# Kernel optimization log

Hardware: AMD Instinct MI355X
Metric: run time of the kernel (lower is better)

Reference implementation:

```python
import jax, jax.numpy as jnp
import numpy as np

B, K, W = 16, 64, 2048
D, DH, DFF, NL, V = 512, 256, 2048, 4, 32001
LN_EPS = 1e-5


def _ln(x, g, b):
    mu = jnp.mean(x, axis=-1, keepdims=True)
    var = jnp.mean(jnp.square(x - mu), axis=-1, keepdims=True)
    return (x - mu) * jax.lax.rsqrt(var + LN_EPS) * g + b


def setup_inputs() -> dict:
    key = jax.random.key(0)
    ks = iter(jax.random.split(key, 64))
    nrm = lambda shape, s=0.02: (jax.random.normal(next(ks), shape, dtype=jnp.float32) * s)
    inp = {
        "cache": jax.random.randint(next(ks), (B, K), 0, V),
        "seq": jax.random.randint(next(ks), (B, W), 0, V),
        "item_embed": nrm((V, D)),
        "cache_pos_embed": nrm((K, D)),
        "seq_pos_embed": nrm((W, D)),
        "segment_embed": nrm((2, D)),
        # per-layer stacked params (leading dim NL)
        "wq_s": nrm((NL, D, DH)), "wk_s": nrm((NL, D, DH)), "wv_s": nrm((NL, D, DH)),
        "wq_c": nrm((NL, D, DH)), "wk_c": nrm((NL, D, DH)), "wv_c": nrm((NL, D, DH)),
        "w_out": nrm((NL, D, D)), "b_out": jnp.zeros((NL, D), jnp.float32),
        "ln1_g": jnp.ones((NL, D), jnp.float32), "ln1_b": jnp.zeros((NL, D), jnp.float32),
        "ln2_g": jnp.ones((NL, D), jnp.float32), "ln2_b": jnp.zeros((NL, D), jnp.float32),
        "w_ff1": nrm((NL, D, DFF)), "b_ff1": jnp.zeros((NL, DFF), jnp.float32),
        "w_ff2": nrm((NL, DFF, D)), "b_ff2": jnp.zeros((NL, D), jnp.float32),
        "fin_g": jnp.ones((D,), jnp.float32), "fin_b": jnp.zeros((D,), jnp.float32),
        "w_ev": nrm((D, 1)), "b_ev": jnp.zeros((1,), jnp.float32),
    }
    return inp


def _forward(cache, seq, item_embed, cache_pos_embed, seq_pos_embed, segment_embed,
             wq_s, wk_s, wv_s, wq_c, wk_c, wv_c, w_out, b_out,
             ln1_g, ln1_b, ln2_g, ln2_b, w_ff1, b_ff1, w_ff2, b_ff2,
             fin_g, fin_b, w_ev, b_ev):
    scale = 1.0 / jnp.sqrt(jnp.float32(DH))
    cache_emb = item_embed[cache] + cache_pos_embed[None, :, :] + segment_embed[0]
    seq_emb = item_embed[seq] + seq_pos_embed[None, :, :] + segment_embed[1]
    h = jnp.concatenate([cache_emb, seq_emb], axis=1)  # (B, K+W, D)
    L = K + W
    # additive mask for stream a: cache rows attend to all seq tokens,
    # seq rows are causal within the window.  (L, W)
    causal = jnp.triu(jnp.full((W, W), -jnp.inf, dtype=jnp.float32), k=1)
    mask_a = jnp.concatenate([jnp.zeros((K, W), jnp.float32), causal], axis=0)

    for l in range(NL):
        hn = _ln(h, ln1_g[l], ln1_b[l])
        hn_seq = hn[:, K:]
        hn_cache = hn[:, :K]
        # stream a: all tokens query the sequence window (causal for seq rows)
        q_a = hn @ wq_s[l]
        k_a = hn_seq @ wk_s[l]
        v_a = hn_seq @ wv_s[l]
        scores_a = jnp.einsum('bld,bwd->blw', q_a, k_a) * scale + mask_a
        out_a = jnp.einsum('blw,bwd->bld', jax.nn.softmax(scores_a, axis=-1), v_a)
        # stream b: all tokens query the cache slots (full attention)
        q_b = hn @ wq_c[l]
        k_b = hn_cache @ wk_c[l]
        v_b = hn_cache @ wv_c[l]
        scores_b = jnp.einsum('bld,bkd->blk', q_b, k_b) * scale
        out_b = jnp.einsum('blk,bkd->bld', jax.nn.softmax(scores_b, axis=-1), v_b)
        attn_out = jnp.concatenate([out_a, out_b], axis=-1)  # (B, L, D)
        h = h + attn_out @ w_out[l] + b_out[l]
        hn2 = _ln(h, ln2_g[l], ln2_b[l])
        h = h + jax.nn.relu(hn2 @ w_ff1[l] + b_ff1[l]) @ w_ff2[l] + b_ff2[l]

    h = _ln(h, fin_g, fin_b)
    logits = (h[:, :K] @ w_ev + b_ev)[..., 0]  # (B, K)
    return logits


def reference(cache, seq, item_embed, cache_pos_embed, seq_pos_embed, segment_embed,
              wq_s, wk_s, wv_s, wq_c, wk_c, wv_c, w_out, b_out,
              ln1_g, ln1_b, ln2_g, ln2_b, w_ff1, b_ff1, w_ff2, b_ff2,
              fin_g, fin_b, w_ev, b_ev):
    return _forward(cache, seq, item_embed, cache_pos_embed, seq_pos_embed, segment_embed,
                    wq_s, wk_s, wv_s, wq_c, wk_c, wv_c, w_out, b_out,
                    ln1_g, ln1_b, ln2_g, ln2_b, w_ff1, b_ff1, w_ff2, b_ff2,
                    fin_g, fin_b, w_ev, b_ev)
```

## Files before the change

### kernel.cpp

```cpp
#include <hip/hip_runtime.h>
#include <hip/hip_bf16.h>
#include <cstdint>

#define CB 16
#define CK 64
#define CW 2048
#define CL 2112
#define CD 512
#define CDH 256
#define CDFF 2048
#define CNL 4
#define CROWS (CB*CL)
#define NCH 2
#define RCH2 (CROWS/NCH)

typedef __attribute__((ext_vector_type(8))) short bf16x8;
typedef __attribute__((ext_vector_type(4))) float f32x4;

__device__ __forceinline__ float bf2f(unsigned short u) {
    union { unsigned int i; float f; } x; x.i = ((unsigned int)u) << 16; return x.f;
}

__device__ __forceinline__ void load_lds16(const void* g, void* l) {
    __builtin_amdgcn_global_load_lds(
        (const __attribute__((address_space(1))) void*)g,
        (__attribute__((address_space(3))) void*)l, 16, 0, 0);
}

__device__ __forceinline__ void xcd_swizzle(int& bx, int& by) {
    const int gx = gridDim.x, nwg = gx * gridDim.y;
    if ((nwg & 7) == 0) {
        const int flat = by * gx + bx;
        const int cpx = nwg >> 3;
        const int swz = (flat & 7) * cpx + (flat >> 3);
        bx = swz % gx; by = swz / gx;
    }
}

#define BM 128
#define BN 128
#define BKG 64

__global__ __launch_bounds__(256) void gemm_bt(
    const short* __restrict__ A, const short* __restrict__ Bt, void* __restrict__ C,
    const float* __restrict__ bias, int M, int N, int Kd,
    int lda, int ldb, int ldc, long sA, long sB, long sC, float scale, int epi,
    int ksplit)
{
    __shared__ short lA[2][BM * BKG];
    __shared__ short lB[2][BN * BKG];
    const int tid = threadIdx.x;
    const int wave = tid >> 6, lane = tid & 63;
    const int wy = wave >> 1, wx = wave & 1;
    const int lr = lane & 15, quad = lane >> 4;
    int bx = blockIdx.x, by = blockIdx.y;
    xcd_swizzle(bx, by);
    const int m0 = by * BM, n0 = bx * BN;
    const int z = blockIdx.z;
    const short* Ab = A + (size_t)z * sA;
    const short* Bb = Bt + (size_t)z * sB;

    f32x4 acc[4][4];
#pragma unroll
    for (int i = 0; i < 4; i++)
#pragma unroll
        for (int j = 0; j < 4; j++) acc[i][j] = (f32x4){0.f, 0.f, 0.f, 0.f};

    const int sRow = lane >> 3;
    const int sCol = (((lane & 7) ^ sRow) << 3);

    int kbeg = 0, kend = Kd;
    if (ksplit > 1) { const int kc = Kd / ksplit; kbeg = z * kc; kend = kbeg + kc; }
    const int nsteps = (kend - kbeg) / BKG;

    auto stage = [&](int buf, int k0) {
#pragma unroll
        for (int n = 0; n < 4; ++n) {
            const int c = wave * 4 + n;
            int ar = m0 + c * 8 + sRow; if (ar > M - 1) ar = M - 1;
            load_lds16(Ab + (size_t)ar * lda + k0 + sCol, &lA[buf][c * 512]);
            int br = n0 + c * 8 + sRow; if (br > N - 1) br = N - 1;
            load_lds16(Bb + (size_t)br * ldb + k0 + sCol, &lB[buf][c * 512]);
        }
    };

    stage(0, kbeg);
    for (int t = 0; t < nsteps; ++t) {
        const int cur = t & 1;
        if (t + 1 < nsteps) {
            stage(cur ^ 1, kbeg + (t + 1) * BKG);
            asm volatile("s_waitcnt vmcnt(8)\n\ts_barrier" ::: "memory");
        } else {
            asm volatile("s_waitcnt vmcnt(0)\n\ts_barrier" ::: "memory");
        }
#pragma unroll
        for (int kk = 0; kk < BKG; kk += 32) {
            const int k4 = kk >> 3;
            bf16x8 av[4], bv[4];
#pragma unroll
            for (int i = 0; i < 4; i++) {
                const int ri = wy * 64 + i * 16 + lr;
                av[i] = *(const bf16x8*)&lA[cur][ri * BKG + ((((k4 + quad) ^ (ri & 7)) << 3))];
            }
#pragma unroll
            for (int j = 0; j < 4; j++) {
                const int rj = wx * 64 + j * 16 + lr;
                bv[j] = *(const bf16x8*)&lB[cur][rj * BKG + ((((k4 + quad) ^ (rj & 7)) << 3))];
            }
#pragma unroll
            for (int i = 0; i < 4; i++)
#pragma unroll
                for (int j = 0; j < 4; j++)
                    acc[i][j] = __builtin_amdgcn_mfma_f32_16x16x32_bf16(av[i], bv[j], acc[i][j], 0, 0, 0);
        }
        asm volatile("s_barrier" ::: "memory");
    }

    const int colBase = n0 + wx * 64 + lr;
    if (epi == 3) {
        float* Cp = (float*)C + (size_t)z * sC;
#pragma unroll
        for (int i = 0; i < 4; i++) {
            const int row0 = m0 + wy * 64 + i * 16 + quad * 4;
#pragma unroll
            for (int j = 0; j < 4; j++) {
                const int col = colBase + j * 16;
                if (col >= N) continue;
                const float bv_ = bias ? bias[col] : 0.f;
#pragma unroll
                for (int r = 0; r < 4; r++) {
                    const int row = row0 + r;
                    if (row < M) Cp[(size_t)row * ldc + col] += acc[i][j][r] + bv_;
                }
            }
        }
    } else {
        __hip_bfloat16* Cp = (__hip_bfloat16*)C + (size_t)z * sC;
#pragma unroll
        for (int i = 0; i < 4; i++) {
            const int row0 = m0 + wy * 64 + i * 16 + quad * 4;
#pragma unroll
            for (int j = 0; j < 4; j++) {
                const int col = colBase + j * 16;
                if (col >= N) continue;
                const float bv_ = (epi == 1) ? bias[col] : 0.f;
#pragma unroll
                for (int r = 0; r < 4; r++) {
                    const int row = row0 + r;
                    if (row < M) {
                        float v = acc[i][j][r];
                        if (epi == 1) { v += bv_; v = v > 0.f ? v : 0.f; }
                        else if (epi == 2) v *= scale;
                        Cp[(size_t)row * ldc + col] = __float2bfloat16(v);
                    }
                }
            }
        }
    }
}

__global__ __launch_bounds__(256, 2) void flash_a(
    const short* __restrict__ q,
    const short* __restrict__ ka,
    const short* __restrict__ vt,
    short* __restrict__ out)
{
    __shared__ short kbuf[64 * 256];
    __shared__ short vbuf[256 * 64];
    __shared__ short pbuf[64 * 64];
    const int tid = threadIdx.x, wave = tid >> 6, lane = tid & 63;
    const int lr = lane & 15, quad = lane >> 4;

    const int id = blockIdx.x;
    const int x = id & 7, k = id >> 3;
    const int b = 2 * x + (k >= 33);
    const int mi = (k >= 33) ? (k - 33) : k;
    const int mt = (mi == 0) ? 0 : (33 - mi);
    const int m0 = mt * 64;
    const short* kab = ka + (size_t)b * 2048 * 256;
    const short* vtb = vt + (size_t)b * 256 * 2048;

    const int nkt = (mt == 0) ? 32 : mt;

    bf16x8 qf[8];
    {
        const int qr = m0 + wave * 16 + lr;
        const short* p0 = q + ((size_t)b * CL + qr) * 512;
#pragma unroll
        for (int s = 0; s < 8; ++s) qf[s] = *(const bf16x8*)(p0 + s * 32 + quad * 8);
    }

    auto stageK = [&](int kt) {
#pragma unroll
        for (int u = 0; u < 8; ++u) {
            const int seg = u * 4 + wave;
            const int idx = seg * 64 + lane;
            const int row = idx >> 5, cp = idx & 31;
            const int cs = cp ^ (row & 7);
            load_lds16(kab + (size_t)(kt * 64 + row) * 256 + cs * 8, kbuf + seg * 512);
        }
    };
    auto stageV = [&](int kt) {
#pragma unroll
        for (int u = 0; u < 8; ++u) {
            const int seg = u * 4 + wave;
            const int idx = seg * 64 + lane;
            const int row = idx >> 3, cp = idx & 7;
            const int cs = cp ^ (row & 7);
            load_lds16(vtb + (size_t)row * 2048 + kt * 64 + cs * 8, vbuf + seg * 512);
        }
    };

    f32x4 acc_o[16];
#pragma unroll
    for (int jd = 0; jd < 16; jd++) acc_o[jd] = (f32x4){0.f, 0.f, 0.f, 0.f};
    float m_run[4], l_run[4];
    int limit[4];
#pragma unroll
    for (int rr = 0; rr < 4; rr++) {
        m_run[rr] = -1e30f; l_run[rr] = 0.f;
        const int trow = m0 + wave * 16 + quad * 4 + rr;
        limit[rr] = (trow < CK) ? CW : (trow - (CK - 1));
    }

    for (int kt = 0; kt < nkt; ++kt) {
        stageK(kt);
        stageV(kt);
        __syncthreads();

        f32x4 s_[4];
#pragma unroll
        for (int j = 0; j < 4; j++) s_[j] = (f32x4){0.f, 0.f, 0.f, 0.f};
#pragma unroll
        for (int s = 0; s < 8; ++s) {
#pragma unroll
            for (int j = 0; j < 4; ++j) {
                const int rj = j * 16 + lr;
                const bf16x8 bv = *(const bf16x8*)&kbuf[rj * 256 + (((s * 4 + quad) ^ (rj & 7)) << 3)];
                s_[j] = __builtin_amdgcn_mfma_f32_16x16x32_bf16(qf[s], bv, s_[j], 0, 0, 0);
            }
        }

        const int kbase = kt * 64;
        float tmax[4];
#pragma unroll
        for (int rr = 0; rr < 4; rr++) tmax[rr] = -1e30f;
#pragma unroll
        for (int j = 0; j < 4; j++) {
            const int key = kbase + j * 16 + lr;
#pragma unroll
            for (int rr = 0; rr < 4; rr++) {
                const float v = (key < limit[rr]) ? s_[j][rr] * 0.0625f : -1e30f;
                s_[j][rr] = v;
                tmax[rr] = fmaxf(tmax[rr], v);
            }
        }
#pragma unroll
        for (int rr = 0; rr < 4; rr++) {
#pragma unroll
            for (int off = 1; off < 16; off <<= 1)
                tmax[rr] = fmaxf(tmax[rr], __shfl_xor(tmax[rr], off));
        }
        float scal[4], rowsum[4];
#pragma unroll
        for (int rr = 0; rr < 4; rr++) {
            const float mn = fmaxf(m_run[rr], tmax[rr]);
            scal[rr] = __expf(m_run[rr] - mn);
            m_run[rr] = mn;
            rowsum[rr] = 0.f;
        }
#pragma unroll
        for (int j = 0; j < 4; j++) {
            const int cch = j * 2 + (lr >> 3);
#pragma unroll
            for (int rr = 0; rr < 4; rr++) {
                const float e = __expf(s_[j][rr] - m_run[rr]);
                rowsum[rr] += e;
                const float eo = __shfl_xor(e, 1);
                const __hip_bfloat16 b0 = __float2bfloat16(e);
                const __hip_bfloat16 b1 = __float2bfloat16(eo);
                const unsigned pk = ((unsigned)(*(const unsigned short*)&b1) << 16)
                                  | (unsigned)(*(const unsigned short*)&b0);
                if (!(lane & 1)) {
                    const int prow = wave * 16 + quad * 4 + rr;
                    *(unsigned*)&pbuf[prow * 64 + ((cch ^ (prow & 7)) << 3) + (lr & 6)] = pk;
                }
            }
        }
#pragma unroll
        for (int rr = 0; rr < 4; rr++) {
#pragma unroll
            for (int off = 1; off < 16; off <<= 1)
                rowsum[rr] += __shfl_xor(rowsum[rr], off);
            l_run[rr] = l_run[rr] * scal[rr] + rowsum[rr];
        }
#pragma unroll
        for (int jd = 0; jd < 16; jd++)
#pragma unroll
            for (int rr = 0; rr < 4; rr++) acc_o[jd][rr] *= scal[rr];


        const int pr = wave * 16 + lr;
#pragma unroll
        for (int s2 = 0; s2 < 2; ++s2) {
            const bf16x8 pa = *(const bf16x8*)&pbuf[pr * 64 + (((s2 * 4 + quad) ^ (pr & 7)) << 3)];
#pragma unroll
            for (int jd = 0; jd < 16; ++jd) {
                const int rj = jd * 16 + lr;
                const bf16x8 bv = *(const bf16x8*)&vbuf[rj * 64 + (((s2 * 4 + quad) ^ (rj & 7)) << 3)];
                acc_o[jd] = __builtin_amdgcn_mfma_f32_16x16x32_bf16(pa, bv, acc_o[jd], 0, 0, 0);
            }
        }
        __syncthreads();
    }

#pragma unroll
    for (int rr = 0; rr < 4; rr++) {
        const int trow = m0 + wave * 16 + quad * 4 + rr;
        const float rinv = 1.f / l_run[rr];
        __hip_bfloat16* op = (__hip_bfloat16*)out + ((size_t)b * CL + trow) * CD;
#pragma unroll
        for (int jd = 0; jd < 16; jd++)
            op[jd * 16 + lr] = __float2bfloat16(acc_o[jd][rr] * rinv);
    }
}

__global__ void embed_kernel(const int* __restrict__ cache, const int* __restrict__ seq,
                             const float* __restrict__ item, const float* __restrict__ cpos,
                             const float* __restrict__ spos, const float* __restrict__ seg,
                             float* __restrict__ h)
{
    const int row = blockIdx.x;
    const int b = row / CL, t = row - b * CL;
    const int d = threadIdx.x * 4;
    int id; const float* pos; const float* sg;
    if (t < CK) { id = cache[b * CK + t]; pos = cpos + (size_t)t * CD; sg = seg; }
    else { const int tt = t - CK; id = seq[b * CW + tt]; pos = spos + (size_t)tt * CD; sg = seg + CD; }
    const float4 ev = *(const float4*)(item + (size_t)id * CD + d);
    const float4 pv = *(const float4*)(pos + d);
    const float4 sv = *(const float4*)(sg + d);
    float4 r; r.x = ev.x + pv.x + sv.x; r.y = ev.y + pv.y + sv.y;
    r.z = ev.z + pv.z + sv.z; r.w = ev.w + pv.w + sv.w;
    *(float4*)(h + (size_t)row * CD + d) = r;
}

__global__ __launch_bounds__(256) void ln_kernel(const float* __restrict__ h, const float* __restrict__ g,
                                                 const float* __restrict__ bb, __hip_bfloat16* __restrict__ out)
{
    const int row = blockIdx.x;
    const float* x = h + (size_t)row * CD;
    const int tid = threadIdx.x, wv = tid >> 6, lane = tid & 63;
    const float2 v = *(const float2*)(x + tid * 2);
    float s = v.x + v.y, s2 = v.x * v.x + v.y * v.y;
    __shared__ float red[8];
#pragma unroll
    for (int off = 32; off; off >>= 1) { s += __shfl_down(s, off); s2 += __shfl_down(s2, off); }
    if (lane == 0) { red[wv] = s; red[4 + wv] = s2; }
    __syncthreads();
    s = red[0] + red[1] + red[2] + red[3];
    s2 = red[4] + red[5] + red[6] + red[7];
    const float mu = s * (1.f / CD);
    const float var = s2 * (1.f / CD) - mu * mu;
    const float rs = rsqrtf(var + 1e-5f);
    const float2 gg = *(const float2*)(g + tid * 2);
    const float2 bv = *(const float2*)(bb + tid * 2);
    out[(size_t)row * CD + tid * 2 + 0] = __float2bfloat16((v.x - mu) * rs * gg.x + bv.x);
    out[(size_t)row * CD + tid * 2 + 1] = __float2bfloat16((v.y - mu) * rs * gg.y + bv.y);
}

__global__ __launch_bounds__(256) void softmax_b_kernel(__hip_bfloat16* __restrict__ sb)
{
    const int row = blockIdx.x * 4 + (threadIdx.x >> 6);
    const int lane = threadIdx.x & 63;
    __hip_bfloat16* pr = sb + (size_t)row * 64;
    float x = __bfloat162float(pr[lane]);
    float m = x;
#pragma unroll
    for (int off = 32; off; off >>= 1) m = fmaxf(m, __shfl_xor(m, off));
    const float e = __expf(x - m);
    float s = e;
#pragma unroll
    for (int off = 32; off; off >>= 1) s += __shfl_xor(s, off);
    pr[lane] = __float2bfloat16(e / s);
}

__global__ __launch_bounds__(256) void final_kernel(const float* __restrict__ h, const float* __restrict__ g,
                                                    const float* __restrict__ bb, const float* __restrict__ wev,
                                                    const float* __restrict__ bev, float* __restrict__ out)
{
    const int idx = blockIdx.x;
    const int b = idx >> 6, t = idx & 63;
    const float* x = h + ((size_t)b * CL + t) * CD;
    const int tid = threadIdx.x, wv = tid >> 6, lane = tid & 63;
    const float2 v = *(const float2*)(x + tid * 2);
    float s = v.x + v.y, s2 = v.x * v.x + v.y * v.y;
    __shared__ float red[8];
#pragma unroll
    for (int off = 32; off; off >>= 1) { s += __shfl_down(s, off); s2 += __shfl_down(s2, off); }
    if (lane == 0) { red[wv] = s; red[4 + wv] = s2; }
    __syncthreads();
    s = red[0] + red[1] + red[2] + red[3];
    s2 = red[4] + red[5] + red[6] + red[7];
    const float mu = s * (1.f / CD);
    const float var = s2 * (1.f / CD) - mu * mu;
    const float rs = rsqrtf(var + 1e-5f);
    const float2 gg = *(const float2*)(g + tid * 2);
    const float2 bv = *(const float2*)(bb + tid * 2);
    const float2 wv2 = *(const float2*)(wev + tid * 2);
    float val = ((v.x - mu) * rs * gg.x + bv.x) * wv2.x + ((v.y - mu) * rs * gg.y + bv.y) * wv2.y;
#pragma unroll
    for (int off = 32; off; off >>= 1) val += __shfl_down(val, off);
    __syncthreads();
    if (lane == 0) red[wv] = val;
    __syncthreads();
    if (tid == 0) out[idx] = red[0] + red[1] + red[2] + red[3] + bev[0];
}

__global__ void transpose_f32(const float* __restrict__ in, __hip_bfloat16* __restrict__ out,
                              int R, int Cc, long inzs, long outzs)
{
    __shared__ float tile[32][33];
    const size_t zi = (size_t)blockIdx.z * inzs;
    const size_t zo = (size_t)blockIdx.z * outzs;
    const int c0 = blockIdx.x * 32, r0 = blockIdx.y * 32;
    const int tx = threadIdx.x, ty = threadIdx.y;
#pragma unroll
    for (int i = ty; i < 32; i += 8)
        tile[i][tx] = in[zi + (size_t)(r0 + i) * Cc + c0 + tx];
    __syncthreads();
#pragma unroll
    for (int i = ty; i < 32; i += 8)
        out[zo + (size_t)(c0 + i) * R + r0 + tx] = __float2bfloat16(tile[tx][i]);
}

extern "C" void kernel_launch(void* const* d_in, const int* in_sizes, int n_in,
                              void* d_out, int out_size, void* d_ws, size_t ws_size,
                              hipStream_t stream)
{
    const int*   cache = (const int*)d_in[0];
    const int*   seq   = (const int*)d_in[1];
    const float* item  = (const float*)d_in[2];
    const float* cpos  = (const float*)d_in[3];
    const float* spos  = (const float*)d_in[4];
    const float* seg   = (const float*)d_in[5];
    const float* wq_s  = (const float*)d_in[6];
    const float* wk_s  = (const float*)d_in[7];
    const float* wv_s  = (const float*)d_in[8];
    const float* wq_c  = (const float*)d_in[9];
    const float* wk_c  = (const float*)d_in[10];
    const float* wv_c  = (const float*)d_in[11];
    const float* w_out = (const float*)d_in[12];
    const float* b_out = (const float*)d_in[13];
    const float* ln1_g = (const float*)d_in[14];
    const float* ln1_b = (const float*)d_in[15];
    const float* ln2_g = (const float*)d_in[16];
    const float* ln2_b = (const float*)d_in[17];
    const float* w_ff1 = (const float*)d_in[18];
    const float* b_ff1 = (const float*)d_in[19];
    const float* w_ff2 = (const float*)d_in[20];
    const float* b_ff2 = (const float*)d_in[21];
    const float* fin_g = (const float*)d_in[22];
    const float* fin_b = (const float*)d_in[23];
    const float* w_ev  = (const float*)d_in[24];
    const float* b_ev  = (const float*)d_in[25];

    char* p = (char*)d_ws;
    auto alloc = [&](size_t bytes) { char* r = p; p += (bytes + 255) & ~(size_t)255; return (void*)r; };
    float* h    = (float*)alloc((size_t)CROWS * CD * 4);
    short* hnat = (short*)alloc((size_t)CROWS * CD * 2);
    short* q    = (short*)alloc((size_t)CROWS * 512 * 2);
    short* ka   = (short*)alloc((size_t)CB * CW * CDH * 2);
    short* vt   = (short*)alloc((size_t)CB * CDH * CW * 2);
    short* kb   = (short*)alloc((size_t)CB * 64 * CDH * 2);
    short* vbT  = (short*)alloc((size_t)CB * CDH * 64 * 2);
    short* sb   = (short*)alloc((size_t)CB * CL * 64 * 2);
    short* big  = (short*)alloc((size_t)4 * CL * CW * 2);
    short* wqT  = (short*)alloc((size_t)CNL * 512 * CD * 2);
    short* wksT = (short*)alloc((size_t)CNL * CDH * CD * 2);
    short* wvsT = (short*)alloc((size_t)CNL * CDH * CD * 2);
    short* wkcT = (short*)alloc((size_t)CNL * CDH * CD * 2);
    short* wvcT = (short*)alloc((size_t)CNL * CDH * CD * 2);
    short* woT  = (short*)alloc((size_t)CNL * CD * CD * 2);
    short* wf1T = (short*)alloc((size_t)CNL * CDFF * CD * 2);
    short* wf2T = (short*)alloc((size_t)CNL * CD * CDFF * 2);
    short* ffbig = q;
    (void)big;

    const dim3 tb(32, 8);
    const long zqk = (long)CD * CDH;
    const long zqT = (long)512 * CD;
    transpose_f32<<<dim3(CDH/32, CD/32, CNL), tb, 0, stream>>>(wq_s, (__hip_bfloat16*)wqT, CD, CDH, zqk, zqT);
    transpose_f32<<<dim3(CDH/32, CD/32, CNL), tb, 0, stream>>>(wq_c, (__hip_bfloat16*)(wqT + (size_t)CDH * CD), CD, CDH, zqk, zqT);
    transpose_f32<<<dim3(CDH/32, CD/32, CNL), tb, 0, stream>>>(wk_s, (__hip_bfloat16*)wksT, CD, CDH, zqk, zqk);
    transpose_f32<<<dim3(CDH/32, CD/32, CNL), tb, 0, stream>>>(wv_s, (__hip_bfloat16*)wvsT, CD, CDH, zqk, zqk);
    transpose_f32<<<dim3(CDH/32, CD/32, CNL), tb, 0, stream>>>(wk_c, (__hip_bfloat16*)wkcT, CD, CDH, zqk, zqk);
    transpose_f32<<<dim3(CDH/32, CD/32, CNL), tb, 0, stream>>>(wv_c, (__hip_bfloat16*)wvcT, CD, CDH, zqk, zqk);
    transpose_f32<<<dim3(CD/32, CD/32, CNL), tb, 0, stream>>>(w_out, (__hip_bfloat16*)woT, CD, CD, (long)CD*CD, (long)CD*CD);
    transpose_f32<<<dim3(CDFF/32, CD/32, CNL), tb, 0, stream>>>(w_ff1, (__hip_bfloat16*)wf1T, CD, CDFF, (long)CD*CDFF, (long)CD*CDFF);
    transpose_f32<<<dim3(CD/32, CDFF/32, CNL), tb, 0, stream>>>(w_ff2, (__hip_bfloat16*)wf2T, CDFF, CD, (long)CD*CDFF, (long)CD*CDFF);

    embed_kernel<<<CROWS, 128, 0, stream>>>(cache, seq, item, cpos, spos, seg, h);

    const int mtilesR = CROWS / 128;
    const int mtilesL = (CL + 127) / 128;

    for (int l = 0; l < CNL; ++l) {
        const short* wqTl  = wqT  + (size_t)l * 512 * CD;
        const short* wksTl = wksT + (size_t)l * CDH * CD;
        const short* wvsTl = wvsT + (size_t)l * CDH * CD;
        const short* wkcTl = wkcT + (size_t)l * CDH * CD;
        const short* wvcTl = wvcT + (size_t)l * CDH * CD;
        const short* woTl  = woT  + (size_t)l * CD * CD;
        const short* wf1Tl = wf1T + (size_t)l * CDFF * CD;
        const short* wf2Tl = wf2T + (size_t)l * CD * CDFF;

        ln_kernel<<<CROWS, 256, 0, stream>>>(h, ln1_g + l * CD, ln1_b + l * CD, (__hip_bfloat16*)hnat);

        gemm_bt<<<dim3(512/128, mtilesR, 1), 256, 0, stream>>>(hnat, wqTl, q, nullptr,
            CROWS, 512, CD, CD, CD, 512, 0, 0, 0, 1.f, 0, 1);
        gemm_bt<<<dim3(CDH/128, CW/128, CB), 256, 0, stream>>>(hnat + (size_t)CK * CD, wksTl, ka, nullptr,
            CW, CDH, CD, CD, CD, CDH, (long)CL * CD, 0, (long)CW * CDH, 1.f, 0, 1);
        gemm_bt<<<dim3(CDH/128, 1, CB), 256, 0, stream>>>(hnat, wkcTl, kb, nullptr,
            64, CDH, CD, CD, CD, CDH, (long)CL * CD, 0, (long)64 * CDH, 1.f, 0, 1);
        gemm_bt<<<dim3(1, CDH/128, CB), 256, 0, stream>>>(wvcTl, hnat, vbT, nullptr,
            CDH, 64, CD, CD, CD, 64, 0, (long)CL * CD, (long)CDH * 64, 1.f, 0, 1);
        gemm_bt<<<dim3(CW/128, CDH/128, CB), 256, 0, stream>>>(wvsTl, hnat + (size_t)CK * CD, vt, nullptr,
            CDH, CW, CD, CD, CD, CW, 0, (long)CL * CD, (long)CDH * CW, 1.f, 0, 1);

        gemm_bt<<<dim3(1, mtilesL, CB), 256, 0, stream>>>(q + CDH, kb, sb, nullptr,
            CL, 64, CDH, 512, CDH, 64, (long)CL * 512, (long)64 * CDH, (long)CL * 64, 0.0625f, 2, 1);
        softmax_b_kernel<<<(CB * CL) / 4, 256, 0, stream>>>((__hip_bfloat16*)sb);
        gemm_bt<<<dim3(CDH/128, mtilesL, CB), 256, 0, stream>>>(sb, vbT, hnat + CDH, nullptr,
            CL, CDH, 64, 64, 64, CD, (long)CL * 64, (long)CDH * 64, (long)CL * CD, 1.f, 0, 1);

        flash_a<<<dim3(528), 256, 0, stream>>>(q, ka, vt, hnat);

        gemm_bt<<<dim3(CD/128, mtilesR, 1), 256, 0, stream>>>(hnat, woTl, h, b_out + l * CD,
            CROWS, CD, CD, CD, CD, CD, 0, 0, 0, 1.f, 3, 1);

        ln_kernel<<<CROWS, 256, 0, stream>>>(h, ln2_g + l * CD, ln2_b + l * CD, (__hip_bfloat16*)hnat);

        for (int c = 0; c < NCH; ++c) {
            const size_t r0 = (size_t)c * RCH2;
            gemm_bt<<<dim3(CDFF/128, RCH2/128, 1), 256, 0, stream>>>(hnat + r0 * CD, wf1Tl, ffbig, b_ff1 + l * CDFF,
                RCH2, CDFF, CD, CD, CD, CDFF, 0, 0, 0, 1.f, 1, 1);
            gemm_bt<<<dim3(CD/128, RCH2/128, 1), 256, 0, stream>>>(ffbig, wf2Tl, h + r0 * CD, b_ff2 + l * CD,
                RCH2, CD, CDFF, CDFF, CDFF, CD, 0, 0, 0, 1.f, 3, 1);
        }
    }

    final_kernel<<<CB * CK, 256, 0, stream>>>(h, fin_g, fin_b, w_ev, b_ev, (float*)d_out);
}
```

Before: 3.420 ms.

## Enlarge flash attention query tile to 128 rows per block for K/V reuse

Each flash_a block now handles 128 query rows instead of 64, with every wave computing two 16-row sub-tiles that share each K and V fragment read from LDS. This halves the number of K/V tile loads per query row and the grid shrinks from 528 to 272 blocks. In exchange, register pressure roughly doubles (two accumulator sets), so launch bounds drop to one block per SM. The coarser causal tiles also do more masked work and leave fewer blocks to balance across CUs.

```diff
diff --git a/kernel.cpp b/kernel.cpp
--- a/kernel.cpp
+++ b/kernel.cpp
@@ -159,7 +159,7 @@
     }
 }
 
-__global__ __launch_bounds__(256, 2) void flash_a(
+__global__ __launch_bounds__(256, 1) void flash_a(
     const short* __restrict__ q,
     const short* __restrict__ ka,
     const short* __restrict__ vt,
@@ -167,27 +167,31 @@
 {
     __shared__ short kbuf[64 * 256];
     __shared__ short vbuf[256 * 64];
-    __shared__ short pbuf[64 * 64];
+    __shared__ short pbuf[128 * 64];
     const int tid = threadIdx.x, wave = tid >> 6, lane = tid & 63;
     const int lr = lane & 15, quad = lane >> 4;
 
     const int id = blockIdx.x;
     const int x = id & 7, k = id >> 3;
-    const int b = 2 * x + (k >= 33);
-    const int mi = (k >= 33) ? (k - 33) : k;
-    const int mt = (mi == 0) ? 0 : (33 - mi);
-    const int m0 = mt * 64;
+    const int b = 2 * x + (k >= 17);
+    const int mi = (k >= 17) ? (k - 17) : k;
+    const int mt = (mi == 0) ? 0 : (17 - mi);
+    const int m0 = mt * 128;
     const short* kab = ka + (size_t)b * 2048 * 256;
     const short* vtb = vt + (size_t)b * 256 * 2048;
 
-    const int nkt = (mt == 0) ? 32 : mt;
-
-    bf16x8 qf[8];
-    {
-        const int qr = m0 + wave * 16 + lr;
+    const int maxr = (m0 + 127 < CL - 1) ? (m0 + 127) : (CL - 1);
+    int nkt = (mt == 0) ? 32 : (maxr >> 6);
+    if (nkt > 32) nkt = 32;
+
+    bf16x8 qf[2][8];
+#pragma unroll
+    for (int i = 0; i < 2; ++i) {
+        int qr = m0 + wave * 32 + i * 16 + lr;
+        if (qr > CL - 1) qr = CL - 1;
         const short* p0 = q + ((size_t)b * CL + qr) * 512;
 #pragma unroll
-        for (int s = 0; s < 8; ++s) qf[s] = *(const bf16x8*)(p0 + s * 32 + quad * 8);
+        for (int s = 0; s < 8; ++s) qf[i][s] = *(const bf16x8*)(p0 + s * 32 + quad * 8);
     }
 
     auto stageK = [&](int kt) {
@@ -211,118 +215,144 @@
         }
     };
 
-    f32x4 acc_o[16];
-#pragma unroll
-    for (int jd = 0; jd < 16; jd++) acc_o[jd] = (f32x4){0.f, 0.f, 0.f, 0.f};
-    float m_run[4], l_run[4];
-    int limit[4];
-#pragma unroll
-    for (int rr = 0; rr < 4; rr++) {
-        m_run[rr] = -1e30f; l_run[rr] = 0.f;
-        const int trow = m0 + wave * 16 + quad * 4 + rr;
-        limit[rr] = (trow < CK) ? CW : (trow - (CK - 1));
-    }
+    f32x4 acc_o[2][16];
+#pragma unroll
+    for (int i = 0; i < 2; i++)
+#pragma unroll
+        for (int jd = 0; jd < 16; jd++) acc_o[i][jd] = (f32x4){0.f, 0.f, 0.f, 0.f};
+    float m_run[2][4], l_run[2][4];
+    int limit[2][4];
+#pragma unroll
+    for (int i = 0; i < 2; i++)
+#pragma unroll
+        for (int rr = 0; rr < 4; rr++) {
+            m_run[i][rr] = -1e30f; l_run[i][rr] = 0.f;
+            const int trow = m0 + wave * 32 + i * 16 + quad * 4 + rr;
+            limit[i][rr] = (trow < CK) ? CW : (trow - (CK - 1));
+        }
 
     for (int kt = 0; kt < nkt; ++kt) {
         stageK(kt);
         stageV(kt);
         __syncthreads();
 
-        f32x4 s_[4];
-#pragma unroll
-        for (int j = 0; j < 4; j++) s_[j] = (f32x4){0.f, 0.f, 0.f, 0.f};
+        f32x4 s_[2][4];
+#pragma unroll
+        for (int i = 0; i < 2; i++)
+#pragma unroll
+            for (int j = 0; j < 4; j++) s_[i][j] = (f32x4){0.f, 0.f, 0.f, 0.f};
 #pragma unroll
         for (int s = 0; s < 8; ++s) {
 #pragma unroll
             for (int j = 0; j < 4; ++j) {
                 const int rj = j * 16 + lr;
                 const bf16x8 bv = *(const bf16x8*)&kbuf[rj * 256 + (((s * 4 + quad) ^ (rj & 7)) << 3)];
-                s_[j] = __builtin_amdgcn_mfma_f32_16x16x32_bf16(qf[s], bv, s_[j], 0, 0, 0);
+                s_[0][j] = __builtin_amdgcn_mfma_f32_16x16x32_bf16(qf[0][s], bv, s_[0][j], 0, 0, 0);
+                s_[1][j] = __builtin_amdgcn_mfma_f32_16x16x32_bf16(qf[1][s], bv, s_[1][j], 0, 0, 0);
             }
         }
 
         const int kbase = kt * 64;
-        float tmax[4];
-#pragma unroll
-        for (int rr = 0; rr < 4; rr++) tmax[rr] = -1e30f;
-#pragma unroll
-        for (int j = 0; j < 4; j++) {
-            const int key = kbase + j * 16 + lr;
+        float tmax[2][4];
+#pragma unroll
+        for (int i = 0; i < 2; i++)
+#pragma unroll
+            for (int rr = 0; rr < 4; rr++) tmax[i][rr] = -1e30f;
+#pragma unroll
+        for (int i = 0; i < 2; i++)
+#pragma unroll
+            for (int j = 0; j < 4; j++) {
+                const int key = kbase + j * 16 + lr;
+#pragma unroll
+                for (int rr = 0; rr < 4; rr++) {
+                    const float v = (key < limit[i][rr]) ? s_[i][j][rr] * 0.0625f : -1e30f;
+                    s_[i][j][rr] = v;
+                    tmax[i][rr] = fmaxf(tmax[i][rr], v);
+                }
+            }
+#pragma unroll
+        for (int i = 0; i < 2; i++)
 #pragma unroll
             for (int rr = 0; rr < 4; rr++) {
-                const float v = (key < limit[rr]) ? s_[j][rr] * 0.0625f : -1e30f;
-                s_[j][rr] = v;
-                tmax[rr] = fmaxf(tmax[rr], v);
-            }
-        }
-#pragma unroll
-        for (int rr = 0; rr < 4; rr++) {
-#pragma unroll
-            for (int off = 1; off < 16; off <<= 1)
-                tmax[rr] = fmaxf(tmax[rr], __shfl_xor(tmax[rr], off));
-        }
-        float scal[4], rowsum[4];
-#pragma unroll
-        for (int rr = 0; rr < 4; rr++) {
-            const float mn = fmaxf(m_run[rr], tmax[rr]);
-            scal[rr] = __expf(m_run[rr] - mn);
-            m_run[rr] = mn;
-            rowsum[rr] = 0.f;
-        }
-#pragma unroll
-        for (int j = 0; j < 4; j++) {
-            const int cch = j * 2 + (lr >> 3);
+#pragma unroll
+                for (int off = 1; off < 16; off <<= 1)
+                    tmax[i][rr] = fmaxf(tmax[i][rr], __shfl_xor(tmax[i][rr], off));
+            }
+        float scal[2][4], rowsum[2][4];
+#pragma unroll
+        for (int i = 0; i < 2; i++)
 #pragma unroll
             for (int rr = 0; rr < 4; rr++) {
-                const float e = __expf(s_[j][rr] - m_run[rr]);
-                rowsum[rr] += e;
-                const float eo = __shfl_xor(e, 1);
-                const __hip_bfloat16 b0 = __float2bfloat16(e);
-                const __hip_bfloat16 b1 = __float2bfloat16(eo);
-                const unsigned pk = ((unsigned)(*(const unsigned short*)&b1) << 16)
-                                  | (unsigned)(*(const unsigned short*)&b0);
-                if (!(lane & 1)) {
-                    const int prow = wave * 16 + quad * 4 + rr;
-                    *(unsigned*)&pbuf[prow * 64 + ((cch ^ (prow & 7)) << 3) + (lr & 6)] = pk;
+                const float mn = fmaxf(m_run[i][rr], tmax[i][rr]);
+                scal[i][rr] = __expf(m_run[i][rr] - mn);
+                m_run[i][rr] = mn;
+                rowsum[i][rr] = 0.f;
+            }
+#pragma unroll
+        for (int i = 0; i < 2; i++)
+#pragma unroll
+            for (int j = 0; j < 4; j++) {
+                const int cch = j * 2 + (lr >> 3);
+#pragma unroll
+                for (int rr = 0; rr < 4; rr++) {
+                    const float e = __expf(s_[i][j][rr] - m_run[i][rr]);
+                    rowsum[i][rr] += e;
+                    const float eo = __shfl_xor(e, 1);
+                    const __hip_bfloat16 b0 = __float2bfloat16(e);
+                    const __hip_bfloat16 b1 = __float2bfloat16(eo);
+                    const unsigned pk = ((unsigned)(*(const unsigned short*)&b1) << 16)
+                                      | (unsigned)(*(const unsigned short*)&b0);
+                    if (!(lane & 1)) {
+                        const int prow = wave * 32 + i * 16 + quad * 4 + rr;
+                        *(unsigned*)&pbuf[prow * 64 + ((cch ^ (prow & 7)) << 3) + (lr & 6)] = pk;
+                    }
                 }
             }
-        }
-#pragma unroll
-        for (int rr = 0; rr < 4; rr++) {
-#pragma unroll
-            for (int off = 1; off < 16; off <<= 1)
-                rowsum[rr] += __shfl_xor(rowsum[rr], off);
-            l_run[rr] = l_run[rr] * scal[rr] + rowsum[rr];
-        }
-#pragma unroll
-        for (int jd = 0; jd < 16; jd++)
-#pragma unroll
-            for (int rr = 0; rr < 4; rr++) acc_o[jd][rr] *= scal[rr];
-
-
-        const int pr = wave * 16 + lr;
+#pragma unroll
+        for (int i = 0; i < 2; i++)
+#pragma unroll
+            for (int rr = 0; rr < 4; rr++) {
+#pragma unroll
+                for (int off = 1; off < 16; off <<= 1)
+                    rowsum[i][rr] += __shfl_xor(rowsum[i][rr], off);
+                l_run[i][rr] = l_run[i][rr] * scal[i][rr] + rowsum[i][rr];
+            }
+#pragma unroll
+        for (int i = 0; i < 2; i++)
+#pragma unroll
+            for (int jd = 0; jd < 16; jd++)
+#pragma unroll
+                for (int rr = 0; rr < 4; rr++) acc_o[i][jd][rr] *= scal[i][rr];
+
+
+        const int pr0 = wave * 32 + lr, pr1 = pr0 + 16;
 #pragma unroll
         for (int s2 = 0; s2 < 2; ++s2) {
-            const bf16x8 pa = *(const bf16x8*)&pbuf[pr * 64 + (((s2 * 4 + quad) ^ (pr & 7)) << 3)];
+            const bf16x8 pa0 = *(const bf16x8*)&pbuf[pr0 * 64 + (((s2 * 4 + quad) ^ (pr0 & 7)) << 3)];
+            const bf16x8 pa1 = *(const bf16x8*)&pbuf[pr1 * 64 + (((s2 * 4 + quad) ^ (pr1 & 7)) << 3)];
 #pragma unroll
             for (int jd = 0; jd < 16; ++jd) {
                 const int rj = jd * 16 + lr;
                 const bf16x8 bv = *(const bf16x8*)&vbuf[rj * 64 + (((s2 * 4 + quad) ^ (rj & 7)) << 3)];
-                acc_o[jd] = __builtin_amdgcn_mfma_f32_16x16x32_bf16(pa, bv, acc_o[jd], 0, 0, 0);
+                acc_o[0][jd] = __builtin_amdgcn_mfma_f32_16x16x32_bf16(pa0, bv, acc_o[0][jd], 0, 0, 0);
+                acc_o[1][jd] = __builtin_amdgcn_mfma_f32_16x16x32_bf16(pa1, bv, acc_o[1][jd], 0, 0, 0);
             }
         }
         __syncthreads();
     }
 
 #pragma unroll
-    for (int rr = 0; rr < 4; rr++) {
-        const int trow = m0 + wave * 16 + quad * 4 + rr;
-        const float rinv = 1.f / l_run[rr];
-        __hip_bfloat16* op = (__hip_bfloat16*)out + ((size_t)b * CL + trow) * CD;
-#pragma unroll
-        for (int jd = 0; jd < 16; jd++)
-            op[jd * 16 + lr] = __float2bfloat16(acc_o[jd][rr] * rinv);
-    }
+    for (int i = 0; i < 2; i++)
+#pragma unroll
+        for (int rr = 0; rr < 4; rr++) {
+            const int trow = m0 + wave * 32 + i * 16 + quad * 4 + rr;
+            if (trow >= CL) continue;
+            const float rinv = 1.f / l_run[i][rr];
+            __hip_bfloat16* op = (__hip_bfloat16*)out + ((size_t)b * CL + trow) * CD;
+#pragma unroll
+            for (int jd = 0; jd < 16; jd++)
+                op[jd * 16 + lr] = __float2bfloat16(acc_o[i][jd][rr] * rinv);
+        }
 }
 
 __global__ void embed_kernel(const int* __restrict__ cache, const int* __restrict__ seq,
@@ -533,7 +563,7 @@
         gemm_bt<<<dim3(CDH/128, mtilesL, CB), 256, 0, stream>>>(sb, vbT, hnat + CDH, nullptr,
             CL, CDH, 64, 64, 64, CD, (long)CL * 64, (long)CDH * 64, (long)CL * CD, 1.f, 0, 1);
 
-        flash_a<<<dim3(528), 256, 0, stream>>>(q, ka, vt, hnat);
+        flash_a<<<dim3(272), 256, 0, stream>>>(q, ka, vt, hnat);
 
         gemm_bt<<<dim3(CD/128, mtilesR, 1), 256, 0, stream>>>(hnat, woTl, h, b_out + l * CD,
             CROWS, CD, CD, CD, CD, CD, 0, 0, 0, 1.f, 3, 1);
```

Measured after the change: 3.827 ms. 1.12x slower.
